# Optimization experiments

Hardware: AMD Instinct MI355X
Metric: run time of the kernel (lower is better)

## Reference

```python
import jax, jax.numpy as jnp
import numpy as np

B, S, D, H, DEPTH, VOCAB = 4096, 64, 512, 8, 4, 2
HD = D // H
EPS = 1e-5


def setup_inputs() -> dict:
    key = jax.random.key(0)
    ks = jax.random.split(key, 12)
    sc = 0.02
    return {
        "a_seq": jax.random.randint(ks[0], (B, S), 0, VOCAB, dtype=jnp.int32),
        "b_seq": jax.random.randint(ks[1], (B, S), 0, VOCAB, dtype=jnp.int32),
        "bit_emb": jax.random.normal(ks[2], (VOCAB, D), jnp.float32),
        "start_state": jax.random.normal(ks[3], (D,), jnp.float32),
        "ln1_g": jnp.ones((DEPTH, D), jnp.float32),
        "ln1_b": jnp.zeros((DEPTH, D), jnp.float32),
        # weights stored [in, out] (transpose of torch nn.Linear layout)
        "qkv_w": jax.random.normal(ks[4], (DEPTH, D, 3 * D), jnp.float32) * sc,
        "qkv_b": jnp.zeros((DEPTH, 3 * D), jnp.float32),
        "out_w": jax.random.normal(ks[5], (DEPTH, D, D), jnp.float32) * sc,
        "out_b": jnp.zeros((DEPTH, D), jnp.float32),
        "ln2_g": jnp.ones((DEPTH, D), jnp.float32),
        "ln2_b": jnp.zeros((DEPTH, D), jnp.float32),
        "ff1_w": jax.random.normal(ks[6], (DEPTH, D, 4 * D), jnp.float32) * sc,
        "ff1_b": jnp.zeros((DEPTH, 4 * D), jnp.float32),
        "ff2_w": jax.random.normal(ks[7], (DEPTH, 4 * D, D), jnp.float32) * sc,
        "ff2_b": jnp.zeros((DEPTH, D), jnp.float32),
        "head_w": jax.random.normal(ks[8], (D, 2), jnp.float32) * sc,
        "head_b": jnp.zeros((2,), jnp.float32),
    }


def _ln(x, g, b):
    m = x.mean(-1, keepdims=True)
    c = x - m
    v = (c * c).mean(-1, keepdims=True)
    return c * jax.lax.rsqrt(v + EPS) * g + b


def reference(a_seq, b_seq, bit_emb, start_state, ln1_g, ln1_b, qkv_w, qkv_b,
              out_w, out_b, ln2_g, ln2_b, ff1_w, ff1_b, ff2_w, ff2_b,
              head_w, head_b):
    # [B,S,D] combined bit embeddings, then time-major for scan
    emb = bit_emb[a_seq] + bit_emb[b_seq]
    xs = jnp.swapaxes(emb, 0, 1)  # [S,B,D]
    h0 = jnp.broadcast_to(start_state, (a_seq.shape[0], D))

    def step(h, xt):
        x = xt + h  # current_input = emb_a + emb_b + h_t, [B,D] (seq_len=1 squeezed)
        for l in range(DEPTH):  # pre-norm TransformerEncoderLayer, norm_first=True
            y = _ln(x, ln1_g[l], ln1_b[l])
            qkv = y @ qkv_w[l] + qkv_b[l]
            # self-attention over a single token: softmax of one score == 1,
            # so the attention output is exactly V (grads to Q,K are zero, as in torch)
            v = qkv[:, 2 * D:]
            x = x + v @ out_w[l] + out_b[l]
            y = _ln(x, ln2_g[l], ln2_b[l])
            x = x + jax.nn.relu(y @ ff1_w[l] + ff1_b[l]) @ ff2_w[l] + ff2_b[l]
        return x, x @ head_w + head_b

    _, logits = jax.lax.scan(step, h0, xs)  # [S,B,2]
    return jnp.swapaxes(logits, 0, 1)  # [B,S,2]
```

## Files before the change

### kernel.cpp

```cpp
#include <hip/hip_runtime.h>
#include <hip/hip_bf16.h>
#include <stdint.h>
#include <stddef.h>

#define B_ 4096
#define S_ 64
#define D_ 512
#define DEPTH_ 4


typedef __attribute__((ext_vector_type(8))) __bf16 bf16x8;
typedef __attribute__((ext_vector_type(4))) float f32x4;
typedef __hip_bfloat16 bf16_t;

constexpr int SPLITZ = 4;

__device__ __forceinline__ void async_copy16(const void* g, void* lds) {
  __builtin_amdgcn_global_load_lds(
      (const __attribute__((address_space(1))) void*)g,
      (__attribute__((address_space(3))) void*)lds, 16, 0, 0);
}

__device__ __forceinline__ float bf2f(bf16_t h) { return __bfloat162float(h); }

__device__ __forceinline__ void fold_p(float v[8], const bf16_t* pz)
{
  alignas(16) bf16_t t[8];
  *(uint4*)t = *(const uint4*)pz;
#pragma unroll
  for (int i = 0; i < 8; ++i) v[i] += bf2f(t[i]);
}

__device__ __forceinline__ void ln_store(const float v[8],
                                         const float* __restrict__ gamma,
                                         const float* __restrict__ beta,
                                         bf16_t* yrow, int lane)
{
  float s = 0.f, ss = 0.f;
#pragma unroll
  for (int i = 0; i < 8; ++i) { s += v[i]; ss += v[i] * v[i]; }
#pragma unroll
  for (int o = 32; o; o >>= 1) { s += __shfl_xor(s, o); ss += __shfl_xor(ss, o); }
  const float m   = s * (1.f / D_);
  const float inv = rsqrtf(ss * (1.f / D_) - m * m + 1e-5f);
  const int c0 = lane * 8;
  float g[8], b[8];
  *(float4*)&g[0] = *(const float4*)&gamma[c0];
  *(float4*)&g[4] = *(const float4*)&gamma[c0 + 4];
  *(float4*)&b[0] = *(const float4*)&beta[c0];
  *(float4*)&b[4] = *(const float4*)&beta[c0 + 4];
  alignas(16) bf16_t o8[8];
#pragma unroll
  for (int i = 0; i < 8; ++i)
    o8[i] = __float2bfloat16((v[i] - m) * inv * g[i] + b[i]);
  *(uint4*)&yrow[c0] = *(const uint4*)o8;
}

template<int TM, int TN, int EPI, int SPLITK>
__launch_bounds__(256)
__global__ void gemm_bf16(const bf16_t* __restrict__ A,
                          const bf16_t* __restrict__ Bt,
                          const float* __restrict__ bias,
                          bf16_t* __restrict__ O,
                          int M, int N, int K)
{
  constexpr int BK  = 64;
  constexpr int WM  = TM / 2, WN = TN / 2;
  constexpr int NMI = WM / 16, NNI = WN / 16;
  constexpr int CA  = TM / 8, CB = TN / 8;
  static_assert(TM * TN <= (TM + TN) * BK, "C tile must fit in staging LDS");

  __shared__ __align__(16) bf16_t smem[(TM + TN) * BK];
  bf16_t* sA = smem;
  bf16_t* sB = smem + TM * BK;

  const int tid  = threadIdx.x;
  const int lane = tid & 63;
  const int wave = tid >> 6;
  const int wm   = wave & 1;
  const int wn   = wave >> 1;
  const int m0   = blockIdx.x * TM;
  const int n0   = blockIdx.y * TN;
  const int KS   = K / SPLITK;
  const int kbeg = blockIdx.z * KS;

  const int lr = lane >> 3;
  const int lc = (lane & 7) * 8;

  f32x4 acc[NMI][NNI];
#pragma unroll
  for (int mi = 0; mi < NMI; ++mi)
#pragma unroll
    for (int ni = 0; ni < NNI; ++ni)
      acc[mi][ni] = (f32x4){0.f, 0.f, 0.f, 0.f};

  for (int k0 = kbeg; k0 < kbeg + KS; k0 += BK) {
#pragma unroll
    for (int c = wave; c < CA; c += 4) {
      const bf16_t* g = A + (size_t)(m0 + c * 8 + lr) * K + (k0 + lc);
      async_copy16(g, (char*)sA + c * 1024);
    }
#pragma unroll
    for (int c = wave; c < CB; c += 4) {
      const bf16_t* g = Bt + (size_t)(n0 + c * 8 + lr) * K + (k0 + lc);
      async_copy16(g, (char*)sB + c * 1024);
    }
    __syncthreads();

#pragma unroll
    for (int kk = 0; kk < BK; kk += 32) {
      bf16x8 af[NMI], bfv[NNI];
#pragma unroll
      for (int mi = 0; mi < NMI; ++mi)
        af[mi] = *(const bf16x8*)&sA[(wm * WM + mi * 16 + (lane & 15)) * BK + kk + (lane >> 4) * 8];
#pragma unroll
      for (int ni = 0; ni < NNI; ++ni)
        bfv[ni] = *(const bf16x8*)&sB[(wn * WN + ni * 16 + (lane & 15)) * BK + kk + (lane >> 4) * 8];
#pragma unroll
      for (int mi = 0; mi < NMI; ++mi)
#pragma unroll
        for (int ni = 0; ni < NNI; ++ni)
          acc[mi][ni] = __builtin_amdgcn_mfma_f32_16x16x32_bf16(af[mi], bfv[ni], acc[mi][ni], 0, 0, 0);
    }
    __syncthreads();
  }

  bf16_t* sC = smem;
#pragma unroll
  for (int mi = 0; mi < NMI; ++mi) {
#pragma unroll
    for (int ni = 0; ni < NNI; ++ni) {
      const int col  = wn * WN + ni * 16 + (lane & 15);
      const int row0 = wm * WM + mi * 16 + ((lane >> 4) << 2);
      const float bv = (SPLITK == 1 || blockIdx.z == 0) ? bias[n0 + col] : 0.f;
#pragma unroll
      for (int r = 0; r < 4; ++r) {
        float v = acc[mi][ni][r] + bv;
        if constexpr (EPI == 1) v = v > 0.f ? v : 0.f;
        sC[(row0 + r) * TN + col] = __float2bfloat16(v);
      }
    }
  }
  __syncthreads();
  bf16_t* Ob = O + (EPI == 2 ? (size_t)blockIdx.z * M * N : (size_t)0);
#pragma unroll
  for (int p = 0; p < (TM * TN) / 2048; ++p) {
    const int chunk = p * 256 + tid;
    const int rr = chunk / (TN / 8);
    const int cc = (chunk % (TN / 8)) * 8;
    *(uint4*)&Ob[(size_t)(m0 + rr) * N + n0 + cc] = *(const uint4*)&sC[rr * TN + cc];
  }
}

__global__ void ln_sum1_kernel(float* __restrict__ X,
                               const bf16_t* __restrict__ P,
                               const float* __restrict__ gamma,
                               const float* __restrict__ beta,
                               bf16_t* __restrict__ Y)
{
  const int row  = blockIdx.x * 4 + (threadIdx.x >> 6);
  const int lane = threadIdx.x & 63;
  const int c0 = lane * 8;
  float* xr = X + (size_t)row * D_;
  float v[8];
  *(float4*)&v[0] = *(const float4*)&xr[c0];
  *(float4*)&v[4] = *(const float4*)&xr[c0 + 4];
  fold_p(v, P + (size_t)row * D_ + c0);
  *(float4*)&xr[c0]     = *(const float4*)&v[0];
  *(float4*)&xr[c0 + 4] = *(const float4*)&v[4];
  ln_store(v, gamma, beta, Y + (size_t)row * D_, lane);
}

__launch_bounds__(256)
__global__ void lnfold_gemm(const float* __restrict__ Xin,
                            const bf16_t* __restrict__ P,
                            float* __restrict__ Xout,
                            const float* __restrict__ gamma,
                            const float* __restrict__ beta,
                            const bf16_t* __restrict__ Bt,
                            const float* __restrict__ bias,
                            bf16_t* __restrict__ O)
{
  constexpr int TM = 32, TN = 128, BK = 64;
  __shared__ __align__(16) bf16_t sY[TM * D_];
  __shared__ __align__(16) bf16_t sB[TN * BK];

  const int tid  = threadIdx.x;
  const int lane = tid & 63;
  const int wave = tid >> 6;
  const int m0   = blockIdx.x * TM;
  const int n0   = blockIdx.y * TN;
  const int c0   = lane * 8;

#pragma unroll
  for (int i = 0; i < 8; ++i) {
    const int row  = wave * 8 + i;
    const int grow = m0 + row;
    const float* xr = Xin + (size_t)grow * D_ + c0;
    float v[8];
    *(float4*)&v[0] = *(const float4*)&xr[0];
    *(float4*)&v[4] = *(const float4*)&xr[4];
#pragma unroll
    for (int z = 0; z < SPLITZ; ++z)
      fold_p(v, P + (size_t)z * B_ * D_ + (size_t)grow * D_ + c0);
    if (blockIdx.y == 0) {
      float* xo = Xout + (size_t)grow * D_ + c0;
      *(float4*)&xo[0] = *(const float4*)&v[0];
      *(float4*)&xo[4] = *(const float4*)&v[4];
    }
    ln_store(v, gamma, beta, &sY[row * D_], lane);
  }

  f32x4 acc[2][2];
#pragma unroll
  for (int mi = 0; mi < 2; ++mi)
#pragma unroll
    for (int ni = 0; ni < 2; ++ni)
      acc[mi][ni] = (f32x4){0.f, 0.f, 0.f, 0.f};

  const int lr = lane >> 3;
  const int lc = (lane & 7) * 8;
  for (int k0 = 0; k0 < D_; k0 += BK) {
#pragma unroll
    for (int c = wave; c < TN / 8; c += 4) {
      const bf16_t* g = Bt + (size_t)(n0 + c * 8 + lr) * D_ + (k0 + lc);
      async_copy16(g, (char*)sB + c * 1024);
    }
    __syncthreads();
#pragma unroll
    for (int kk = 0; kk < BK; kk += 32) {
      bf16x8 af[2], bfv[2];
#pragma unroll
      for (int mi = 0; mi < 2; ++mi)
        af[mi] = *(const bf16x8*)&sY[(mi * 16 + (lane & 15)) * D_ + k0 + kk + (lane >> 4) * 8];
#pragma unroll
      for (int ni = 0; ni < 2; ++ni)
        bfv[ni] = *(const bf16x8*)&sB[(wave * 32 + ni * 16 + (lane & 15)) * BK + kk + (lane >> 4) * 8];
#pragma unroll
      for (int mi = 0; mi < 2; ++mi)
#pragma unroll
        for (int ni = 0; ni < 2; ++ni)
          acc[mi][ni] = __builtin_amdgcn_mfma_f32_16x16x32_bf16(af[mi], bfv[ni], acc[mi][ni], 0, 0, 0);
    }
    __syncthreads();
  }

  bf16_t* sC = sY;
#pragma unroll
  for (int mi = 0; mi < 2; ++mi) {
#pragma unroll
    for (int ni = 0; ni < 2; ++ni) {
      const int col  = wave * 32 + ni * 16 + (lane & 15);
      const int row0 = mi * 16 + ((lane >> 4) << 2);
      const float bv = bias[n0 + col];
#pragma unroll
      for (int r = 0; r < 4; ++r)
        sC[(row0 + r) * TN + col] = __float2bfloat16(acc[mi][ni][r] + bv);
    }
  }
  __syncthreads();
#pragma unroll
  for (int p = 0; p < (TM * TN) / 2048; ++p) {
    const int chunk = p * 256 + tid;
    const int rr = chunk / (TN / 8);
    const int cc = (chunk % (TN / 8)) * 8;
    *(uint4*)&O[(size_t)(m0 + rr) * D_ + n0 + cc] = *(const uint4*)&sC[rr * TN + cc];
  }
}

__launch_bounds__(256)
__global__ void addln_gemm(const int* __restrict__ a_seq,
                           const int* __restrict__ b_seq,
                           const float* __restrict__ bit_emb,
                           const float* __restrict__ hsrc, int hstride,
                           const bf16_t* __restrict__ P,
                           float* __restrict__ Xout,
                           const float* __restrict__ gamma,
                           const float* __restrict__ beta,
                           const bf16_t* __restrict__ Bt,
                           const float* __restrict__ bias,
                           bf16_t* __restrict__ O,
                           int t,
                           const float* __restrict__ hw,
                           const float* __restrict__ hb,
                           float* __restrict__ out)
{
  constexpr int TM = 32, TN = 128, BK = 64;
  __shared__ __align__(16) bf16_t sY[TM * D_];
  __shared__ __align__(16) bf16_t sB[TN * BK];

  const int tid  = threadIdx.x;
  const int lane = tid & 63;
  const int wave = tid >> 6;
  const int m0   = blockIdx.x * TM;
  const int n0   = blockIdx.y * TN;
  const int c0   = lane * 8;

  const bool do_head = (out != nullptr) && (blockIdx.y == 0);
  float w[16];
  if (do_head) {
#pragma unroll
    for (int i = 0; i < 4; ++i)
      *(float4*)&w[i * 4] = *(const float4*)&hw[lane * 16 + i * 4];
  }

#pragma unroll
  for (int i = 0; i < 8; ++i) {
    const int row  = wave * 8 + i;
    const int grow = m0 + row;
    const int ai = a_seq[grow * S_ + t];
    const int bi = b_seq[grow * S_ + t];
    const float* pr = hsrc + (size_t)grow * hstride + c0;
    float p[8];
    *(float4*)&p[0] = *(const float4*)&pr[0];
    *(float4*)&p[4] = *(const float4*)&pr[4];
    if (P != nullptr) {
#pragma unroll
      for (int z = 0; z < SPLITZ; ++z)
        fold_p(p, P + (size_t)z * B_ * D_ + (size_t)grow * D_ + c0);
    }
    if (do_head) {
      float s0 = 0.f, s1 = 0.f;
#pragma unroll
      for (int j = 0; j < 8; ++j) { s0 += p[j] * w[2 * j]; s1 += p[j] * w[2 * j + 1]; }
#pragma unroll
      for (int o = 32; o; o >>= 1) { s0 += __shfl_xor(s0, o); s1 += __shfl_xor(s1, o); }
      if (lane == 0) {
        float* po = out + (size_t)grow * (S_ * 2) + (t - 1) * 2;
        po[0] = s0 + hb[0];
        po[1] = s1 + hb[1];
      }
    }
    float ea[8], eb[8], v[8];
    *(float4*)&ea[0] = *(const float4*)&bit_emb[ai * D_ + c0];
    *(float4*)&ea[4] = *(const float4*)&bit_emb[ai * D_ + c0 + 4];
    *(float4*)&eb[0] = *(const float4*)&bit_emb[bi * D_ + c0];
    *(float4*)&eb[4] = *(const float4*)&bit_emb[bi * D_ + c0 + 4];
#pragma unroll
    for (int j = 0; j < 8; ++j) v[j] = ea[j] + eb[j] + p[j];
    if (blockIdx.y == 0) {
      float* xo = Xout + (size_t)grow * D_ + c0;
      *(float4*)&xo[0] = *(const float4*)&v[0];
      *(float4*)&xo[4] = *(const float4*)&v[4];
    }
    ln_store(v, gamma, beta, &sY[row * D_], lane);
  }

  f32x4 acc[2][2];
#pragma unroll
  for (int mi = 0; mi < 2; ++mi)
#pragma unroll
    for (int ni = 0; ni < 2; ++ni)
      acc[mi][ni] = (f32x4){0.f, 0.f, 0.f, 0.f};

  const int lr = lane >> 3;
  const int lc = (lane & 7) * 8;
  for (int k0 = 0; k0 < D_; k0 += BK) {
#pragma unroll
    for (int c = wave; c < TN / 8; c += 4) {
      const bf16_t* g = Bt + (size_t)(n0 + c * 8 + lr) * D_ + (k0 + lc);
      async_copy16(g, (char*)sB + c * 1024);
    }
    __syncthreads();
#pragma unroll
    for (int kk = 0; kk < BK; kk += 32) {
      bf16x8 af[2], bfv[2];
#pragma unroll
      for (int mi = 0; mi < 2; ++mi)
        af[mi] = *(const bf16x8*)&sY[(mi * 16 + (lane & 15)) * D_ + k0 + kk + (lane >> 4) * 8];
#pragma unroll
      for (int ni = 0; ni < 2; ++ni)
        bfv[ni] = *(const bf16x8*)&sB[(wave * 32 + ni * 16 + (lane & 15)) * BK + kk + (lane >> 4) * 8];
#pragma unroll
      for (int mi = 0; mi < 2; ++mi)
#pragma unroll
        for (int ni = 0; ni < 2; ++ni)
          acc[mi][ni] = __builtin_amdgcn_mfma_f32_16x16x32_bf16(af[mi], bfv[ni], acc[mi][ni], 0, 0, 0);
    }
    __syncthreads();
  }

  bf16_t* sC = sY;
#pragma unroll
  for (int mi = 0; mi < 2; ++mi) {
#pragma unroll
    for (int ni = 0; ni < 2; ++ni) {
      const int col  = wave * 32 + ni * 16 + (lane & 15);
      const int row0 = mi * 16 + ((lane >> 4) << 2);
      const float bv = bias[n0 + col];
#pragma unroll
      for (int r = 0; r < 4; ++r)
        sC[(row0 + r) * TN + col] = __float2bfloat16(acc[mi][ni][r] + bv);
    }
  }
  __syncthreads();
#pragma unroll
  for (int p = 0; p < (TM * TN) / 2048; ++p) {
    const int chunk = p * 256 + tid;
    const int rr = chunk / (TN / 8);
    const int cc = (chunk % (TN / 8)) * 8;
    *(uint4*)&O[(size_t)(m0 + rr) * D_ + n0 + cc] = *(const uint4*)&sC[rr * TN + cc];
  }
}

__global__ void head_kernel(const float* __restrict__ X,
                            const bf16_t* __restrict__ P,
                            const float* __restrict__ hw,
                            const float* __restrict__ hb,
                            float* __restrict__ out, int t)
{
  const int row  = blockIdx.x * 4 + (threadIdx.x >> 6);
  const int lane = threadIdx.x & 63;
  const float* xr = X + (size_t)row * D_;
  const int c0 = lane * 8;
  float v[8];
  *(float4*)&v[0] = *(const float4*)&xr[c0];
  *(float4*)&v[4] = *(const float4*)&xr[c0 + 4];
#pragma unroll
  for (int z = 0; z < SPLITZ; ++z)
    fold_p(v, P + (size_t)z * B_ * D_ + (size_t)row * D_ + c0);
  float w[16];
#pragma unroll
  for (int i = 0; i < 4; ++i)
    *(float4*)&w[i * 4] = *(const float4*)&hw[lane * 16 + i * 4];
  float s0 = 0.f, s1 = 0.f;
#pragma unroll
  for (int i = 0; i < 8; ++i) { s0 += v[i] * w[2 * i]; s1 += v[i] * w[2 * i + 1]; }
#pragma unroll
  for (int o = 32; o; o >>= 1) { s0 += __shfl_xor(s0, o); s1 += __shfl_xor(s1, o); }
  if (lane == 0) {
    float* po = out + (size_t)row * (S_ * 2) + t * 2;
    po[0] = s0 + hb[0];
    po[1] = s1 + hb[1];
  }
}

__global__ void prep_wc(const float* __restrict__ qkv_w,
                        const float* __restrict__ out_w,
                        float* __restrict__ wc)
{
  const int n = blockIdx.x * 256 + threadIdx.x;
  const int k = blockIdx.y;
  const int l = blockIdx.z;
  const float* qrow = qkv_w + ((size_t)l * D_ + k) * (3 * D_) + 2 * D_;
  const float* ow   = out_w + (size_t)l * D_ * D_;
  float acc = 0.f;
  for (int j = 0; j < D_; ++j) acc += qrow[j] * ow[(size_t)j * D_ + n];
  wc[((size_t)l * D_ + k) * D_ + n] = acc;
}

__global__ void prep_bc(const float* __restrict__ qkv_b,
                        const float* __restrict__ out_w,
                        const float* __restrict__ out_b,
                        float* __restrict__ bc)
{
  const int l = blockIdx.x;
  const int n = threadIdx.x;
  const float* qb = qkv_b + (size_t)l * (3 * D_) + 2 * D_;
  const float* ow = out_w + (size_t)l * D_ * D_;
  float acc = out_b[(size_t)l * D_ + n];
  for (int j = 0; j < D_; ++j) acc += qb[j] * ow[(size_t)j * D_ + n];
  bc[(size_t)l * D_ + n] = acc;
}

__global__ void transpose_conv(const float* __restrict__ src,
                               bf16_t* __restrict__ dst, int R, int C)
{
  __shared__ float tile[32][33];
  const int l = blockIdx.z;
  const float* s = src + (size_t)l * R * C;
  bf16_t* d = dst + (size_t)l * R * C;
  const int c0 = blockIdx.x * 32, r0 = blockIdx.y * 32;
  const int tx = threadIdx.x, ty = threadIdx.y;
  tile[ty][tx] = s[(size_t)(r0 + ty) * C + (c0 + tx)];
  __syncthreads();
  d[(size_t)(c0 + ty) * R + (r0 + tx)] = __float2bfloat16(tile[tx][ty]);
}

extern "C" void kernel_launch(void* const* d_in, const int* in_sizes, int n_in,
                              void* d_out, int out_size, void* d_ws, size_t ws_size,
                              hipStream_t stream)
{
  const int*   a_seq     = (const int*)  d_in[0];
  const int*   b_seq     = (const int*)  d_in[1];
  const float* bit_emb   = (const float*)d_in[2];
  const float* start     = (const float*)d_in[3];
  const float* ln1_g     = (const float*)d_in[4];
  const float* ln1_b     = (const float*)d_in[5];
  const float* qkv_w     = (const float*)d_in[6];
  const float* qkv_b     = (const float*)d_in[7];
  const float* out_w     = (const float*)d_in[8];
  const float* out_b     = (const float*)d_in[9];
  const float* ln2_g     = (const float*)d_in[10];
  const float* ln2_b     = (const float*)d_in[11];
  const float* ff1_w     = (const float*)d_in[12];
  const float* ff1_b     = (const float*)d_in[13];
  const float* ff2_w     = (const float*)d_in[14];
  const float* ff2_b     = (const float*)d_in[15];
  const float* head_w    = (const float*)d_in[16];
  const float* head_b    = (const float*)d_in[17];
  float* out = (float*)d_out;

  char* ws = (char*)d_ws;
  float*  XA    = (float*) ws; ws += (size_t)B_ * D_ * 4;
  float*  XB    = (float*) ws; ws += (size_t)B_ * D_ * 4;
  bf16_t* Y     = (bf16_t*)ws; ws += (size_t)B_ * D_ * 2;
  bf16_t* U     = (bf16_t*)ws; ws += (size_t)B_ * 4 * D_ * 2;
  bf16_t* WCT   = (bf16_t*)ws; ws += (size_t)DEPTH_ * D_ * D_ * 2;
  bf16_t* FF1T  = (bf16_t*)ws; ws += (size_t)DEPTH_ * D_ * 4 * D_ * 2;
  bf16_t* FF2T  = (bf16_t*)ws; ws += (size_t)DEPTH_ * 4 * D_ * D_ * 2;
  float*  BC    = (float*) ws; ws += (size_t)DEPTH_ * D_ * 4;
  float*  WCTMP = (float*) ws; ws += (size_t)DEPTH_ * D_ * D_ * 4;
  bf16_t* PSPL  = (bf16_t*)ws; ws += (size_t)SPLITZ * B_ * D_ * 2;
  bf16_t* P1    = (bf16_t*)ws; ws += (size_t)B_ * D_ * 2;

  prep_wc<<<dim3(2, 512, 4), 256, 0, stream>>>(qkv_w, out_w, WCTMP);
  prep_bc<<<4, 512, 0, stream>>>(qkv_b, out_w, out_b, BC);
  transpose_conv<<<dim3(16, 16, 4),  dim3(32, 32), 0, stream>>>(WCTMP, WCT, 512, 512);
  transpose_conv<<<dim3(64, 16, 4),  dim3(32, 32), 0, stream>>>(ff1_w, FF1T, 512, 2048);
  transpose_conv<<<dim3(16, 64, 4),  dim3(32, 32), 0, stream>>>(ff2_w, FF2T, 2048, 512);

  for (int t = 0; t < S_; ++t) {
    if (t == 0)
      addln_gemm<<<dim3(B_ / 32, 4), 256, 0, stream>>>(
          a_seq, b_seq, bit_emb, start, 0, nullptr, XA,
          ln1_g, ln1_b, WCT, BC, P1, t, head_w, head_b, nullptr);
    else
      addln_gemm<<<dim3(B_ / 32, 4), 256, 0, stream>>>(
          a_seq, b_seq, bit_emb, XB, D_, PSPL, XA,
          ln1_g, ln1_b, WCT, BC, P1, t, head_w, head_b, out);
    float* cur = XA;
    float* alt = XB;
    for (int l = 0; l < DEPTH_; ++l) {
      if (l > 0) {
        lnfold_gemm<<<dim3(B_ / 32, 4), 256, 0, stream>>>(
            cur, PSPL, alt,
            ln1_g + (size_t)l * D_, ln1_b + (size_t)l * D_,
            WCT + (size_t)l * D_ * D_, BC + (size_t)l * D_, P1);
        float* tmp = cur; cur = alt; alt = tmp;
      }
      ln_sum1_kernel<<<B_ / 4, 256, 0, stream>>>(cur, P1,
                                                 ln2_g + (size_t)l * D_,
                                                 ln2_b + (size_t)l * D_, Y);
      gemm_bf16<128, 128, 1, 1><<<dim3(32, 16), 256, 0, stream>>>(
          Y, FF1T + (size_t)l * D_ * 4 * D_, ff1_b + (size_t)l * 4 * D_, U,
          B_, 4 * D_, D_);
      gemm_bf16<128, 128, 2, SPLITZ><<<dim3(32, 4, SPLITZ), 256, 0, stream>>>(
          U, FF2T + (size_t)l * 4 * D_ * D_, ff2_b + (size_t)l * D_, PSPL,
          B_, D_, 4 * D_);
    }
  }
  head_kernel<<<B_ / 4, 256, 0, stream>>>(XB, PSPL, head_w, head_b, out, S_ - 1);
}
```

Baseline: 14.89 ms.

## Load weight fragments directly from global and XOR-swizzle LDS activations

The fused LN+GEMM kernels stop staging weight tiles through LDS with per-chunk barriers. Each wave now reads its B fragments straight from global memory into registers across a fully unrolled K loop. The normalized activation tile in LDS is stored with an XOR swizzle on columns to cut bank conflicts on MFMA fragment reads. This removes many __syncthreads and LDS traffic, but relies on cache hits for the weight reads and adds global-load latency without explicit prefetch.

```diff
diff --git a/kernel.cpp b/kernel.cpp
--- a/kernel.cpp
+++ b/kernel.cpp
@@ -31,10 +31,10 @@
   for (int i = 0; i < 8; ++i) v[i] += bf2f(t[i]);
 }
 
-__device__ __forceinline__ void ln_store(const float v[8],
-                                         const float* __restrict__ gamma,
-                                         const float* __restrict__ beta,
-                                         bf16_t* yrow, int lane)
+__device__ __forceinline__ void ln_vals(const float v[8],
+                                        const float* __restrict__ gamma,
+                                        const float* __restrict__ beta,
+                                        int lane, bf16_t o8[8])
 {
   float s = 0.f, ss = 0.f;
 #pragma unroll
@@ -49,11 +49,30 @@
   *(float4*)&g[4] = *(const float4*)&gamma[c0 + 4];
   *(float4*)&b[0] = *(const float4*)&beta[c0];
   *(float4*)&b[4] = *(const float4*)&beta[c0 + 4];
-  alignas(16) bf16_t o8[8];
 #pragma unroll
   for (int i = 0; i < 8; ++i)
     o8[i] = __float2bfloat16((v[i] - m) * inv * g[i] + b[i]);
-  *(uint4*)&yrow[c0] = *(const uint4*)o8;
+}
+
+__device__ __forceinline__ void ln_store(const float v[8],
+                                         const float* __restrict__ gamma,
+                                         const float* __restrict__ beta,
+                                         bf16_t* yrow, int lane)
+{
+  alignas(16) bf16_t o8[8];
+  ln_vals(v, gamma, beta, lane, o8);
+  *(uint4*)&yrow[lane * 8] = *(const uint4*)o8;
+}
+
+__device__ __forceinline__ void ln_store_swz(const float v[8],
+                                             const float* __restrict__ gamma,
+                                             const float* __restrict__ beta,
+                                             bf16_t* srow, int row, int lane)
+{
+  alignas(16) bf16_t o8[8];
+  ln_vals(v, gamma, beta, lane, o8);
+  const int c0s = (lane * 8) ^ ((row & 7) << 3);
+  *(uint4*)&srow[c0s] = *(const uint4*)o8;
 }
 
 template<int TM, int TN, int EPI, int SPLITK>
@@ -171,6 +190,60 @@
   ln_store(v, gamma, beta, Y + (size_t)row * D_, lane);
 }
 
+__device__ __forceinline__ void small_gemm_loop(const bf16_t* __restrict__ sY,
+                                                const bf16_t* __restrict__ Bt,
+                                                int n0, int wave, int lane,
+                                                f32x4 acc[2][2])
+{
+  const bf16_t* b0 = Bt + (size_t)(n0 + wave * 32 + (lane & 15)) * D_ + (lane >> 4) * 8;
+  const bf16_t* b1 = b0 + (size_t)16 * D_;
+  const int r0 = (lane & 15);
+  const int r1 = 16 + (lane & 15);
+  const int x0 = (r0 & 7) << 3;
+  const int ka = (lane >> 4) * 8;
+#pragma unroll
+  for (int k0 = 0; k0 < D_; k0 += 32) {
+    bf16x8 af0, af1, bv0, bv1;
+    bv0 = *(const bf16x8*)&b0[k0];
+    bv1 = *(const bf16x8*)&b1[k0];
+    af0 = *(const bf16x8*)&sY[r0 * D_ + ((k0 + ka) ^ x0)];
+    af1 = *(const bf16x8*)&sY[r1 * D_ + ((k0 + ka) ^ x0)];
+    acc[0][0] = __builtin_amdgcn_mfma_f32_16x16x32_bf16(af0, bv0, acc[0][0], 0, 0, 0);
+    acc[0][1] = __builtin_amdgcn_mfma_f32_16x16x32_bf16(af0, bv1, acc[0][1], 0, 0, 0);
+    acc[1][0] = __builtin_amdgcn_mfma_f32_16x16x32_bf16(af1, bv0, acc[1][0], 0, 0, 0);
+    acc[1][1] = __builtin_amdgcn_mfma_f32_16x16x32_bf16(af1, bv1, acc[1][1], 0, 0, 0);
+  }
+}
+
+__device__ __forceinline__ void small_gemm_epi(bf16_t* sC, bf16_t* __restrict__ O,
+                                               const float* __restrict__ bias,
+                                               const f32x4 acc[2][2],
+                                               int m0, int n0, int wave, int lane,
+                                               int tid)
+{
+  constexpr int TM = 32, TN = 128;
+#pragma unroll
+  for (int mi = 0; mi < 2; ++mi) {
+#pragma unroll
+    for (int ni = 0; ni < 2; ++ni) {
+      const int col  = wave * 32 + ni * 16 + (lane & 15);
+      const int row0 = mi * 16 + ((lane >> 4) << 2);
+      const float bv = bias[n0 + col];
+#pragma unroll
+      for (int r = 0; r < 4; ++r)
+        sC[(row0 + r) * TN + col] = __float2bfloat16(acc[mi][ni][r] + bv);
+    }
+  }
+  __syncthreads();
+#pragma unroll
+  for (int p = 0; p < (TM * TN) / 2048; ++p) {
+    const int chunk = p * 256 + tid;
+    const int rr = chunk / (TN / 8);
+    const int cc = (chunk % (TN / 8)) * 8;
+    *(uint4*)&O[(size_t)(m0 + rr) * D_ + n0 + cc] = *(const uint4*)&sC[rr * TN + cc];
+  }
+}
+
 __launch_bounds__(256)
 __global__ void lnfold_gemm(const float* __restrict__ Xin,
                             const bf16_t* __restrict__ P,
@@ -181,15 +254,14 @@
                             const float* __restrict__ bias,
                             bf16_t* __restrict__ O)
 {
-  constexpr int TM = 32, TN = 128, BK = 64;
+  constexpr int TM = 32;
   __shared__ __align__(16) bf16_t sY[TM * D_];
-  __shared__ __align__(16) bf16_t sB[TN * BK];
 
   const int tid  = threadIdx.x;
   const int lane = tid & 63;
   const int wave = tid >> 6;
   const int m0   = blockIdx.x * TM;
-  const int n0   = blockIdx.y * TN;
+  const int n0   = blockIdx.y * 128;
   const int c0   = lane * 8;
 
 #pragma unroll
@@ -208,8 +280,9 @@
       *(float4*)&xo[0] = *(const float4*)&v[0];
       *(float4*)&xo[4] = *(const float4*)&v[4];
     }
-    ln_store(v, gamma, beta, &sY[row * D_], lane);
-  }
+    ln_store_swz(v, gamma, beta, &sY[row * D_], row, lane);
+  }
+  __syncthreads();
 
   f32x4 acc[2][2];
 #pragma unroll
@@ -218,54 +291,10 @@
     for (int ni = 0; ni < 2; ++ni)
       acc[mi][ni] = (f32x4){0.f, 0.f, 0.f, 0.f};
 
-  const int lr = lane >> 3;
-  const int lc = (lane & 7) * 8;
-  for (int k0 = 0; k0 < D_; k0 += BK) {
-#pragma unroll
-    for (int c = wave; c < TN / 8; c += 4) {
-      const bf16_t* g = Bt + (size_t)(n0 + c * 8 + lr) * D_ + (k0 + lc);
-      async_copy16(g, (char*)sB + c * 1024);
-    }
-    __syncthreads();
-#pragma unroll
-    for (int kk = 0; kk < BK; kk += 32) {
-      bf16x8 af[2], bfv[2];
-#pragma unroll
-      for (int mi = 0; mi < 2; ++mi)
-        af[mi] = *(const bf16x8*)&sY[(mi * 16 + (lane & 15)) * D_ + k0 + kk + (lane >> 4) * 8];
-#pragma unroll
-      for (int ni = 0; ni < 2; ++ni)
-        bfv[ni] = *(const bf16x8*)&sB[(wave * 32 + ni * 16 + (lane & 15)) * BK + kk + (lane >> 4) * 8];
-#pragma unroll
-      for (int mi = 0; mi < 2; ++mi)
-#pragma unroll
-        for (int ni = 0; ni < 2; ++ni)
-          acc[mi][ni] = __builtin_amdgcn_mfma_f32_16x16x32_bf16(af[mi], bfv[ni], acc[mi][ni], 0, 0, 0);
-    }
-    __syncthreads();
-  }
-
-  bf16_t* sC = sY;
-#pragma unroll
-  for (int mi = 0; mi < 2; ++mi) {
-#pragma unroll
-    for (int ni = 0; ni < 2; ++ni) {
-      const int col  = wave * 32 + ni * 16 + (lane & 15);
-      const int row0 = mi * 16 + ((lane >> 4) << 2);
-      const float bv = bias[n0 + col];
-#pragma unroll
-      for (int r = 0; r < 4; ++r)
-        sC[(row0 + r) * TN + col] = __float2bfloat16(acc[mi][ni][r] + bv);
-    }
-  }
-  __syncthreads();
-#pragma unroll
-  for (int p = 0; p < (TM * TN) / 2048; ++p) {
-    const int chunk = p * 256 + tid;
-    const int rr = chunk / (TN / 8);
-    const int cc = (chunk % (TN / 8)) * 8;
-    *(uint4*)&O[(size_t)(m0 + rr) * D_ + n0 + cc] = *(const uint4*)&sC[rr * TN + cc];
-  }
+  small_gemm_loop(sY, Bt, n0, wave, lane, acc);
+
+  __syncthreads();
+  small_gemm_epi(sY, O, bias, acc, m0, n0, wave, lane, tid);
 }
 
 __launch_bounds__(256)
@@ -285,15 +314,14 @@
                            const float* __restrict__ hb,
                            float* __restrict__ out)
 {
-  constexpr int TM = 32, TN = 128, BK = 64;
+  constexpr int TM = 32;
   __shared__ __align__(16) bf16_t sY[TM * D_];
-  __shared__ __align__(16) bf16_t sB[TN * BK];
 
   const int tid  = threadIdx.x;
   const int lane = tid & 63;
   const int wave = tid >> 6;
   const int m0   = blockIdx.x * TM;
-  const int n0   = blockIdx.y * TN;
+  const int n0   = blockIdx.y * 128;
   const int c0   = lane * 8;
 
   const bool do_head = (out != nullptr) && (blockIdx.y == 0);
@@ -343,8 +371,9 @@
       *(float4*)&xo[0] = *(const float4*)&v[0];
       *(float4*)&xo[4] = *(const float4*)&v[4];
     }
-    ln_store(v, gamma, beta, &sY[row * D_], lane);
-  }
+    ln_store_swz(v, gamma, beta, &sY[row * D_], row, lane);
+  }
+  __syncthreads();
 
   f32x4 acc[2][2];
 #pragma unroll
@@ -353,54 +382,10 @@
     for (int ni = 0; ni < 2; ++ni)
       acc[mi][ni] = (f32x4){0.f, 0.f, 0.f, 0.f};
 
-  const int lr = lane >> 3;
-  const int lc = (lane & 7) * 8;
-  for (int k0 = 0; k0 < D_; k0 += BK) {
-#pragma unroll
-    for (int c = wave; c < TN / 8; c += 4) {
-      const bf16_t* g = Bt + (size_t)(n0 + c * 8 + lr) * D_ + (k0 + lc);
-      async_copy16(g, (char*)sB + c * 1024);
-    }
-    __syncthreads();
-#pragma unroll
-    for (int kk = 0; kk < BK; kk += 32) {
-      bf16x8 af[2], bfv[2];
-#pragma unroll
-      for (int mi = 0; mi < 2; ++mi)
-        af[mi] = *(const bf16x8*)&sY[(mi * 16 + (lane & 15)) * D_ + k0 + kk + (lane >> 4) * 8];
-#pragma unroll
-      for (int ni = 0; ni < 2; ++ni)
-        bfv[ni] = *(const bf16x8*)&sB[(wave * 32 + ni * 16 + (lane & 15)) * BK + kk + (lane >> 4) * 8];
-#pragma unroll
-      for (int mi = 0; mi < 2; ++mi)
-#pragma unroll
-        for (int ni = 0; ni < 2; ++ni)
-          acc[mi][ni] = __builtin_amdgcn_mfma_f32_16x16x32_bf16(af[mi], bfv[ni], acc[mi][ni], 0, 0, 0);
-    }
-    __syncthreads();
-  }
-
-  bf16_t* sC = sY;
-#pragma unroll
-  for (int mi = 0; mi < 2; ++mi) {
-#pragma unroll
-    for (int ni = 0; ni < 2; ++ni) {
-      const int col  = wave * 32 + ni * 16 + (lane & 15);
-      const int row0 = mi * 16 + ((lane >> 4) << 2);
-      const float bv = bias[n0 + col];
-#pragma unroll
-      for (int r = 0; r < 4; ++r)
-        sC[(row0 + r) * TN + col] = __float2bfloat16(acc[mi][ni][r] + bv);
-    }
-  }
-  __syncthreads();
-#pragma unroll
-  for (int p = 0; p < (TM * TN) / 2048; ++p) {
-    const int chunk = p * 256 + tid;
-    const int rr = chunk / (TN / 8);
-    const int cc = (chunk % (TN / 8)) * 8;
-    *(uint4*)&O[(size_t)(m0 + rr) * D_ + n0 + cc] = *(const uint4*)&sC[rr * TN + cc];
-  }
+  small_gemm_loop(sY, Bt, n0, wave, lane, acc);
+
+  __syncthreads();
+  small_gemm_epi(sY, O, bias, acc, m0, n0, wave, lane, tid);
 }
 
 __global__ void head_kernel(const float* __restrict__ X,
```

Measured after the change: 14.75 ms. About the same (-0.9%).
